# Optimization experiments

Measured on AMD Instinct MI355X. Metric: run time of the kernel, lower is better.

## Reference

```python
import jax, jax.numpy as jnp
import numpy as np

# ---- model constants (match init_kwargs) ----
E = 128; GH = 8; GD = E // GH; GL = 3          # graph emb / heads / layers
SH = 4; SD = E // SH; SL = 4                   # sequence transformer
ATOM = 64; BOND = 16; RBF_K = 32; CUTOFF = 5.0
VOCAB = 64; SEQL = 128
N = 32                                          # nodes per graph (equal-size graphs)
GC = 64; GS = 16; BMOL = 16; DEG = 64; GF = 3   # conf graphs / scaffold graphs / molecules / edges-per-graph
LN_EPS = 1e-5
CENTERS = jnp.linspace(0.0, CUTOFF, RBF_K)
GAMMA = (CUTOFF / (RBF_K - 1)) ** -2            # GaussianRBF gamma = (center spacing)^-2


def _ln(x, g, b):
    mu = x.mean(-1, keepdims=True)
    var = ((x - mu) ** 2).mean(-1, keepdims=True)
    return (x - mu) / jnp.sqrt(var + LN_EPS) * g + b


def _graph_encoder(x, edge_index, edge_attr, pos, G, p):
    # node projection
    h = x @ p["gproj_w"] + p["gproj_b"]                      # [G*N, E]
    # edge features: bond features + RBF(distance)
    d = jnp.clip(edge_attr[:, -1], 0.0, 10.0)
    rbf = jnp.exp(-GAMMA * (d[:, None] - CENTERS) ** 2)       # [M, K]
    ef = jnp.concatenate([edge_attr[:, :-1], rbf], axis=1)    # [M, BOND+K]
    # EdgeNetwork: per-edge matrix (gather -> matvec -> scatter-add)
    M = ef.shape[0]
    m = (ef @ p["elin_w"] + p["elin_b"]).reshape(M, E, E)
    msg = jnp.einsum("mef,mf->me", m, h[edge_index[1]])      # [M, E]
    aggr = jnp.zeros_like(h).at[edge_index[0]].add(msg)
    h = _ln(h + aggr, p["eln_g"], p["eln_b"])
    # dense per-graph layout (equal-size graphs -> reshape, mask is all-true)
    hb = h.reshape(G, N, E)
    pp = pos.reshape(G, N, 3)
    d2 = jnp.sum((pp[:, :, None, :] - pp[:, None, :, :]) ** 2, axis=-1)
    dist = jnp.where(d2 > 0, jnp.sqrt(jnp.where(d2 > 0, d2, 1.0)), 0.0)  # safe cdist
    inv_sqrt_d = 1.0 / np.sqrt(GD)
    for l in range(GL):
        def heads(t):
            return t.reshape(G, N, GH, GD).transpose(0, 2, 1, 3)
        q = heads(hb @ p["gt_qw"][l] + p["gt_qb"][l])
        k = heads(hb @ p["gt_kw"][l] + p["gt_kb"][l])
        v = heads(hb @ p["gt_vw"][l] + p["gt_vb"][l])
        s = jnp.einsum("bhnd,bhmd->bhnm", q, k) * inv_sqrt_d + dist[:, None]
        s = jnp.clip(s, -10.0, 10.0)
        a = jax.nn.softmax(s, axis=-1)                       # all nodes valid -> no mask
        o = jnp.einsum("bhnm,bhmd->bhnd", a, v).transpose(0, 2, 1, 3).reshape(G, N, E)
        o = o @ p["gt_ow"][l] + p["gt_ob"][l]
        x1 = _ln(hb + o, p["gt_ln1g"][l], p["gt_ln1b"][l])
        ff = jax.nn.relu(x1 @ p["gt_f1w"][l] + p["gt_f1b"][l]) @ p["gt_f2w"][l] + p["gt_f2b"][l]
        hb = _ln(x1 + ff, p["gt_ln2g"][l], p["gt_ln2b"][l])
    # masked mean pool with the source's eps in the denominator
    return hb.sum(1) / (N + 1e-8)


def _seq_encoder(tokens, p):
    B, L = tokens.shape
    x = p["tok_emb"][tokens] + p["pos_emb"][:L][None]        # [B, L, E]
    inv_sqrt_d = 1.0 / np.sqrt(SD)
    for l in range(SL):
        qkv = x @ p["se_inw"][l] + p["se_inb"][l]            # [B, L, 3E]
        q, k, v = jnp.split(qkv, 3, axis=-1)
        def heads(t):
            return t.reshape(B, L, SH, SD).transpose(0, 2, 1, 3)
        q, k, v = heads(q), heads(k), heads(v)
        a = jax.nn.softmax(jnp.einsum("bhnd,bhmd->bhnm", q, k) * inv_sqrt_d, axis=-1)
        o = jnp.einsum("bhnm,bhmd->bhnd", a, v).transpose(0, 2, 1, 3).reshape(B, L, E)
        o = o @ p["se_ow"][l] + p["se_ob"][l]
        x = _ln(x + o, p["se_ln1g"][l], p["se_ln1b"][l])      # post-norm (torch default)
        ff = jax.nn.relu(x @ p["se_f1w"][l] + p["se_f1b"][l]) @ p["se_f2w"][l] + p["se_f2b"][l]
        x = _ln(x + ff, p["se_ln2g"][l], p["se_ln2b"][l])
    return x.mean(1)                                          # [B, E]


def _forward(p, conf_edge_index, scaf_edge_index, tokens, conf_per_mol):
    g_all = _graph_encoder(p["conf_x"], conf_edge_index, p["conf_edge_attr"], p["conf_pos"], GC, p)
    conf_emb = g_all.reshape(-1, conf_per_mol, E).mean(1)     # per-molecule conformer mean (equal counts)
    scaf_emb = _graph_encoder(p["scaf_x"], scaf_edge_index, p["scaf_edge_attr"], p["scaf_pos"], GS, p)
    total = conf_emb + scaf_emb
    seq = _seq_encoder(tokens, p)
    # FusionGating
    gate_h = jax.nn.relu(jnp.concatenate([total, seq], -1) @ p["fg1_w"] + p["fg1_b"])
    gate = jax.nn.sigmoid(gate_h @ p["fg2_w"] + p["fg2_b"])
    fused = gate * total + (1.0 - gate) * seq
    # CrossModalAttention: MHA over a length-1 sequence (unsqueeze(0)) -> softmax
    # weights are identically 1, so attn(q_in, kv, kv) == out_proj(v_proj(kv)).
    g, s = fused, fused
    for l in range(2):
        g2s = (s @ p["cm_g2s_vw"][l] + p["cm_g2s_vb"][l]) @ p["cm_g2s_ow"][l] + p["cm_g2s_ob"][l]
        g = _ln(g + g2s, p["cm_n1g"][l], p["cm_n1b"][l])
        s2g = (g @ p["cm_s2g_vw"][l] + p["cm_s2g_vb"][l]) @ p["cm_s2g_ow"][l] + p["cm_s2g_ob"][l]
        s = _ln(s + s2g, p["cm_n2g"][l], p["cm_n2b"][l])
    final = (g + s) * 0.5
    comb = jnp.concatenate([final, p["graph_features"]], -1)
    return (jax.nn.relu(comb @ p["r1_w"] + p["r1_b"]) @ p["r2_w"] + p["r2_b"])[:, 0]


def setup_inputs() -> dict:
    ks = iter(jax.random.split(jax.random.key(0), 64))
    def nrm(shape, s):
        return (jax.random.normal(next(ks), shape) * s).astype(jnp.float32)
    inp = {}
    def mk_graph(prefix, G):
        inp[prefix + "_x"] = nrm((G * N, ATOM), 1.0)
        off = (jnp.arange(G) * N)[:, None]
        src = jax.random.randint(next(ks), (G, DEG), 0, N) + off   # within-graph edges
        dst = jax.random.randint(next(ks), (G, DEG), 0, N) + off
        inp[prefix + "_edge_index"] = jnp.stack([src.ravel(), dst.ravel()]).astype(jnp.int32)
        bond = jax.random.uniform(next(ks), (G * DEG, BOND))
        dist = jax.random.uniform(next(ks), (G * DEG, 1), minval=0.5, maxval=CUTOFF)
        inp[prefix + "_edge_attr"] = jnp.concatenate([bond, dist], 1).astype(jnp.float32)
        inp[prefix + "_pos"] = nrm((G * N, 3), 2.0)
    mk_graph("conf", GC)
    mk_graph("scaf", GS)
    inp["tokens"] = jax.random.randint(next(ks), (BMOL, SEQL), 1, VOCAB).astype(jnp.int32)
    inp["graph_features"] = nrm((BMOL, GF), 1.0)
    inp["conf_per_mol"] = GC // BMOL
    W = 0.05
    inp["gproj_w"] = nrm((ATOM, E), W); inp["gproj_b"] = jnp.zeros(E)
    inp["elin_w"] = nrm((BOND + RBF_K, E * E), W); inp["elin_b"] = jnp.zeros(E * E)
    inp["eln_g"] = jnp.ones(E); inp["eln_b"] = jnp.zeros(E)
    for nm in ["qw", "kw", "vw", "ow"]:
        inp["gt_" + nm] = nrm((GL, E, E), W)
        inp["gt_" + nm[0] + "b"] = jnp.zeros((GL, E))
    inp["gt_ln1g"] = jnp.ones((GL, E)); inp["gt_ln1b"] = jnp.zeros((GL, E))
    inp["gt_f1w"] = nrm((GL, E, 2 * E), W); inp["gt_f1b"] = jnp.zeros((GL, 2 * E))
    inp["gt_f2w"] = nrm((GL, 2 * E, E), W); inp["gt_f2b"] = jnp.zeros((GL, E))
    inp["gt_ln2g"] = jnp.ones((GL, E)); inp["gt_ln2b"] = jnp.zeros((GL, E))
    inp["tok_emb"] = nrm((VOCAB, E), 0.02); inp["pos_emb"] = nrm((256, E), 0.02)
    inp["se_inw"] = nrm((SL, E, 3 * E), W); inp["se_inb"] = jnp.zeros((SL, 3 * E))
    inp["se_ow"] = nrm((SL, E, E), W); inp["se_ob"] = jnp.zeros((SL, E))
    inp["se_ln1g"] = jnp.ones((SL, E)); inp["se_ln1b"] = jnp.zeros((SL, E))
    inp["se_f1w"] = nrm((SL, E, 2 * E), W); inp["se_f1b"] = jnp.zeros((SL, 2 * E))
    inp["se_f2w"] = nrm((SL, 2 * E, E), W); inp["se_f2b"] = jnp.zeros((SL, E))
    inp["se_ln2g"] = jnp.ones((SL, E)); inp["se_ln2b"] = jnp.zeros((SL, E))
    inp["fg1_w"] = nrm((2 * E, 64), W); inp["fg1_b"] = jnp.zeros(64)
    inp["fg2_w"] = nrm((64, E), W); inp["fg2_b"] = jnp.zeros(E)
    for nm in ["g2s", "s2g"]:
        inp["cm_" + nm + "_vw"] = nrm((2, E, E), W); inp["cm_" + nm + "_vb"] = jnp.zeros((2, E))
        inp["cm_" + nm + "_ow"] = nrm((2, E, E), W); inp["cm_" + nm + "_ob"] = jnp.zeros((2, E))
    inp["cm_n1g"] = jnp.ones((2, E)); inp["cm_n1b"] = jnp.zeros((2, E))
    inp["cm_n2g"] = jnp.ones((2, E)); inp["cm_n2b"] = jnp.zeros((2, E))
    inp["r1_w"] = nrm((E + GF, E), W); inp["r1_b"] = jnp.zeros(E)
    inp["r2_w"] = nrm((E, 1), W); inp["r2_b"] = jnp.zeros(1)
    return inp


def reference(conf_x, conf_edge_attr, conf_pos, scaf_x, scaf_edge_attr, scaf_pos, graph_features,
              gproj_w, gproj_b, elin_w, elin_b, eln_g, eln_b,
              gt_qw, gt_qb, gt_kw, gt_kb, gt_vw, gt_vb, gt_ow, gt_ob,
              gt_ln1g, gt_ln1b, gt_f1w, gt_f1b, gt_f2w, gt_f2b, gt_ln2g, gt_ln2b,
              tok_emb, pos_emb,
              se_inw, se_inb, se_ow, se_ob, se_ln1g, se_ln1b, se_f1w, se_f1b, se_f2w, se_f2b, se_ln2g, se_ln2b,
              fg1_w, fg1_b, fg2_w, fg2_b,
              cm_g2s_vw, cm_g2s_vb, cm_g2s_ow, cm_g2s_ob, cm_n1g, cm_n1b,
              cm_s2g_vw, cm_s2g_vb, cm_s2g_ow, cm_s2g_ob, cm_n2g, cm_n2b,
              r1_w, r1_b, r2_w, r2_b,
              conf_edge_index, scaf_edge_index, tokens, conf_per_mol):
    p = dict(locals())
    return _forward(p, conf_edge_index, scaf_edge_index, tokens, conf_per_mol)
```

## Files before the change

kernel.cpp:

```cpp
#include <hip/hip_runtime.h>
#include <hip/hip_bf16.h>


__device__ __forceinline__ float blk_norm(float v, int e, float* sred)
{
  float s = v;
  #pragma unroll
  for (int o = 1; o < 64; o <<= 1) s += __shfl_xor(s, o);
  if ((e & 63) == 0) sred[e >> 6] = s;
  __syncthreads();
  float mean = (sred[0] + sred[1]) * (1.0f / 128.0f);
  __syncthreads();
  float d = v - mean;
  float s2 = d * d;
  #pragma unroll
  for (int o = 1; o < 64; o <<= 1) s2 += __shfl_xor(s2, o);
  if ((e & 63) == 0) sred[e >> 6] = s2;
  __syncthreads();
  float var = (sred[0] + sred[1]) * (1.0f / 128.0f);
  __syncthreads();
  return d / sqrtf(var + 1e-5f);
}

__global__ __launch_bounds__(128) void node_proj_k(
    const float* __restrict__ cx, const float* __restrict__ sx,
    const float* __restrict__ w, const float* __restrict__ b,
    float* __restrict__ h, float* __restrict__ aggr)
{
  int r = blockIdx.x, e = threadIdx.x;
  const float* x = (r < 2048) ? (cx + (size_t)r * 64) : (sx + (size_t)(r - 2048) * 64);
  __shared__ float xs[64];
  if (e < 64) xs[e] = x[e];
  __syncthreads();
  float acc = b[e];
  for (int a = 0; a < 64; a++) acc += xs[a] * w[a * 128 + e];
  h[(size_t)r * 128 + e] = acc;
  aggr[(size_t)r * 128 + e] = 0.0f;
}

__global__ __launch_bounds__(256) void dist_k(
    const float* __restrict__ cpos, const float* __restrict__ spos, float* __restrict__ dist)
{
  int g = blockIdx.x, tid = threadIdx.x;
  __shared__ float P[96];
  const float* p = (g < 64) ? (cpos + (size_t)g * 96) : (spos + (size_t)(g - 64) * 96);
  if (tid < 96) P[tid] = p[tid];
  __syncthreads();
  #pragma unroll
  for (int jj = 0; jj < 4; jj++) {
    int idx = tid * 4 + jj;
    int i = idx >> 5, j = idx & 31;
    float dx = P[i * 3 + 0] - P[j * 3 + 0];
    float dy = P[i * 3 + 1] - P[j * 3 + 1];
    float dz = P[i * 3 + 2] - P[j * 3 + 2];
    float d2 = dx * dx + dy * dy + dz * dz;
    dist[(size_t)g * 1024 + idx] = (d2 > 0.0f) ? sqrtf(d2) : 0.0f;
  }
}

__global__ __launch_bounds__(256) void edge_gemm_k(
    const float* __restrict__ cea, const float* __restrict__ sea,
    const int* __restrict__ cei, const int* __restrict__ sei,
    const float* __restrict__ h,
    const float* __restrict__ elw, const float* __restrict__ elb,
    float* __restrict__ aggr)
{
  __shared__ float efs[32][8];
  __shared__ float As[32][36];
  __shared__ float Bs[32][136];
  const int tid = threadIdx.x;
  const int m0 = blockIdx.x * 32;
  const int kt0 = blockIdx.y * 28;
  const int c0 = kt0 >> 2;
  {
    int t = tid >> 3, cc = tid & 7;
    if (cc < 7) {
      int c = c0 + cc;
      int m = m0 + t;
      const float* attr = (m < 4096) ? (cea + (size_t)m * 17) : (sea + (size_t)(m - 4096) * 17);
      float val;
      if (c < 16) val = attr[c];
      else if (c < 48) {
        float d = fminf(fmaxf(attr[16], 0.0f), 10.0f);
        float t2 = d - (float)((c - 16) * (5.0 / 31.0));
        val = expf(-38.44f * t2 * t2);
      } else val = 1.0f;
      efs[t][cc] = val;
    }
  }
  const int gk = tid & 31, gt = (tid >> 5) * 4;
  float hreg[4][4];
  #pragma unroll
  for (int i = 0; i < 4; i++) {
    int m = m0 + gt + i;
    int dst = (m < 4096) ? cei[4096 + m] : (sei[1024 + (m - 4096)] + 2048);
    const float* hp = h + (size_t)dst * 128 + gk;
    hreg[i][0] = hp[0]; hreg[i][1] = hp[32]; hreg[i][2] = hp[64]; hreg[i][3] = hp[96];
  }
  const int tn = tid & 31, tm = tid >> 5;
  const int e0 = 4 * tn, t0 = 4 * tm;
  const int se = tid >> 1, sk = (tid & 1) * 16;
  float acc[4][4] = {};
  __syncthreads();
  #pragma unroll 1
  for (int kt = kt0; kt < kt0 + 28; kt++) {
    int c = kt >> 2, cc = c - c0, j = kt & 3;
    float4 av;
    av.x = efs[gt + 0][cc] * hreg[0][j];
    av.y = efs[gt + 1][cc] * hreg[1][j];
    av.z = efs[gt + 2][cc] * hreg[2][j];
    av.w = efs[gt + 3][cc] * hreg[3][j];
    *(float4*)&As[gk][gt] = av;
    const float* bp = ((c < 48) ? (elw + (size_t)c * 16384) : elb) + (size_t)se * 128 + j * 32 + sk;
    float4 w0 = *(const float4*)(bp + 0);
    float4 w1 = *(const float4*)(bp + 4);
    float4 w2 = *(const float4*)(bp + 8);
    float4 w3 = *(const float4*)(bp + 12);
    Bs[sk + 0][se] = w0.x;  Bs[sk + 1][se] = w0.y;  Bs[sk + 2][se] = w0.z;  Bs[sk + 3][se] = w0.w;
    Bs[sk + 4][se] = w1.x;  Bs[sk + 5][se] = w1.y;  Bs[sk + 6][se] = w1.z;  Bs[sk + 7][se] = w1.w;
    Bs[sk + 8][se] = w2.x;  Bs[sk + 9][se] = w2.y;  Bs[sk + 10][se] = w2.z; Bs[sk + 11][se] = w2.w;
    Bs[sk + 12][se] = w3.x; Bs[sk + 13][se] = w3.y; Bs[sk + 14][se] = w3.z; Bs[sk + 15][se] = w3.w;
    __syncthreads();
    #pragma unroll
    for (int kk = 0; kk < 32; kk++) {
      float4 a = *(const float4*)&As[kk][t0];
      float4 b = *(const float4*)&Bs[kk][e0];
      acc[0][0] += a.x * b.x; acc[0][1] += a.x * b.y; acc[0][2] += a.x * b.z; acc[0][3] += a.x * b.w;
      acc[1][0] += a.y * b.x; acc[1][1] += a.y * b.y; acc[1][2] += a.y * b.z; acc[1][3] += a.y * b.w;
      acc[2][0] += a.z * b.x; acc[2][1] += a.z * b.y; acc[2][2] += a.z * b.z; acc[2][3] += a.z * b.w;
      acc[3][0] += a.w * b.x; acc[3][1] += a.w * b.y; acc[3][2] += a.w * b.z; acc[3][3] += a.w * b.w;
    }
    __syncthreads();
  }
  #pragma unroll
  for (int i = 0; i < 4; i++) {
    int m = m0 + t0 + i;
    int src = (m < 4096) ? cei[m] : (sei[m - 4096] + 2048);
    float* dst = aggr + (size_t)src * 128 + e0;
    atomicAdd(dst + 0, acc[i][0]);
    atomicAdd(dst + 1, acc[i][1]);
    atomicAdd(dst + 2, acc[i][2]);
    atomicAdd(dst + 3, acc[i][3]);
  }
}

__device__ __forceinline__ void gemm16_body(
    const float* __restrict__ A, const float* __restrict__ Bp,
    const float* __restrict__ biasp, float* __restrict__ Cp,
    int row0, int ldb, int ldc)
{
  __shared__ float Sa[32][20];
  __shared__ float Bs[32][136];
  const int tid = threadIdx.x;
  const int tm = tid >> 5, tn = tid & 31;
  const int t0 = 2 * tm, e0 = 4 * tn;
  const int ar = tid >> 4, ak = (tid & 15) * 2;
  const int bk = tid >> 3, be = (tid & 7) * 16;
  float acc[2][4] = {};
  for (int k0 = 0; k0 < 128; k0 += 32) {
    float2 av = *(const float2*)(A + (size_t)(row0 + ar) * 128 + k0 + ak);
    Sa[ak][ar] = av.x; Sa[ak + 1][ar] = av.y;
    const float* bp = Bp + (size_t)(k0 + bk) * ldb + be;
    float4 b0v = *(const float4*)(bp + 0);
    float4 b1v = *(const float4*)(bp + 4);
    float4 b2v = *(const float4*)(bp + 8);
    float4 b3v = *(const float4*)(bp + 12);
    Bs[bk][be + 0] = b0v.x;  Bs[bk][be + 1] = b0v.y;  Bs[bk][be + 2] = b0v.z;  Bs[bk][be + 3] = b0v.w;
    Bs[bk][be + 4] = b1v.x;  Bs[bk][be + 5] = b1v.y;  Bs[bk][be + 6] = b1v.z;  Bs[bk][be + 7] = b1v.w;
    Bs[bk][be + 8] = b2v.x;  Bs[bk][be + 9] = b2v.y;  Bs[bk][be + 10] = b2v.z; Bs[bk][be + 11] = b2v.w;
    Bs[bk][be + 12] = b3v.x; Bs[bk][be + 13] = b3v.y; Bs[bk][be + 14] = b3v.z; Bs[bk][be + 15] = b3v.w;
    __syncthreads();
    #pragma unroll
    for (int kk = 0; kk < 32; kk++) {
      float2 a = *(const float2*)&Sa[kk][t0];
      float4 b = *(const float4*)&Bs[kk][e0];
      acc[0][0] += a.x * b.x; acc[0][1] += a.x * b.y; acc[0][2] += a.x * b.z; acc[0][3] += a.x * b.w;
      acc[1][0] += a.y * b.x; acc[1][1] += a.y * b.y; acc[1][2] += a.y * b.z; acc[1][3] += a.y * b.w;
    }
    __syncthreads();
  }
  #pragma unroll
  for (int i = 0; i < 2; i++) {
    float* cp = Cp + (size_t)(row0 + t0 + i) * ldc + e0;
    #pragma unroll
    for (int j = 0; j < 4; j++) cp[j] = acc[i][j] + biasp[e0 + j];
  }
}

__global__ __launch_bounds__(256) void qkv_k(
    int gBlocks,
    const float* __restrict__ ghb,
    const float* gqw, const float* gkw, const float* gvw,
    const float* gqb, const float* gkb, const float* gvb, float* gout,
    const float* __restrict__ sxs, const float* sw, const float* sb, float* sout)
{
  int bx = blockIdx.x;
  if (bx < gBlocks) {
    int z = bx / 160, rt = bx % 160;
    const float* B = (z == 0) ? gqw : (z == 1) ? gkw : gvw;
    const float* bias = (z == 0) ? gqb : (z == 1) ? gkb : gvb;
    gemm16_body(ghb, B, bias, gout + (size_t)z * 327680, rt * 16, 128, 128);
  } else {
    int i = bx - gBlocks;
    int z = i >> 7, rt = i & 127;
    gemm16_body(sxs, sw + z * 128, sb + z * 128, sout + z * 128, rt * 16, 384, 384);
  }
}

__device__ __forceinline__ void gattn_body(
    int g, int h, const float* __restrict__ q, const float* __restrict__ k,
    const float* __restrict__ v, const float* __restrict__ dist, float* __restrict__ o)
{
  __shared__ float qs[32][17], ksh[32][17], vsh[32][17], ss[32][33], rs[32];
  const int tid = threadIdx.x;
  {
    int idx = tid * 2;
    int i = idx >> 4, d = idx & 15;
    size_t base = ((size_t)(g * 32 + i)) * 128 + h * 16 + d;
    qs[i][d] = q[base];  qs[i][d + 1] = q[base + 1];
    ksh[i][d] = k[base]; ksh[i][d + 1] = k[base + 1];
    vsh[i][d] = v[base]; vsh[i][d + 1] = v[base + 1];
  }
  __syncthreads();
  {
    int i = tid >> 3, j0 = (tid & 7) * 4;
    for (int j = j0; j < j0 + 4; j++) {
      float a = 0;
      #pragma unroll
      for (int d = 0; d < 16; d++) a += qs[i][d] * ksh[j][d];
      a = a * 0.25f + dist[(size_t)g * 1024 + i * 32 + j];
      ss[i][j] = fminf(fmaxf(a, -10.0f), 10.0f);
    }
  }
  __syncthreads();
  if (tid < 32) {
    float m = -1e30f;
    for (int j = 0; j < 32; j++) m = fmaxf(m, ss[tid][j]);
    float sm = 0;
    for (int j = 0; j < 32; j++) { float ex = expf(ss[tid][j] - m); ss[tid][j] = ex; sm += ex; }
    rs[tid] = 1.0f / sm;
  }
  __syncthreads();
  {
    int idx = tid * 2;
    int i = idx >> 4, d = idx & 15;
    float a0 = 0, a1 = 0;
    for (int j = 0; j < 32; j++) { float wj = ss[i][j]; a0 += wj * vsh[j][d]; a1 += wj * vsh[j][d + 1]; }
    float r = rs[i];
    size_t base = ((size_t)(g * 32 + i)) * 128 + h * 16 + d;
    o[base] = a0 * r; o[base + 1] = a1 * r;
  }
}

__device__ __forceinline__ void sattn_body(
    int b, int h, int qt, const float* __restrict__ qkv, float* __restrict__ o)
{
  __shared__ float ks[128][33];
  __shared__ float vs[128][33];
  __shared__ float qs2[32][33];
  __shared__ float ss2[32][129];
  __shared__ float red[32][8];
  __shared__ float red2[32][8];
  const int tid = threadIdx.x;
  {
    int l = tid >> 1, d0 = (tid & 1) * 16;
    const float* kp = qkv + ((size_t)(b * 128 + l)) * 384 + 128 + h * 32 + d0;
    #pragma unroll
    for (int j = 0; j < 16; j++) { ks[l][d0 + j] = kp[j]; vs[l][d0 + j] = kp[128 + j]; }
  }
  {
    int i = tid >> 3, d0 = (tid & 7) * 4;
    const float* qp = qkv + ((size_t)(b * 128 + qt * 32 + i)) * 384 + h * 32 + d0;
    #pragma unroll
    for (int j = 0; j < 4; j++) qs2[i][d0 + j] = qp[j];
  }
  __syncthreads();
  const int i = tid >> 3, sub = tid & 7;
  {
    int j0 = sub * 16;
    for (int j = j0; j < j0 + 16; j++) {
      float a = 0;
      #pragma unroll
      for (int d = 0; d < 32; d++) a += qs2[i][d] * ks[j][d];
      ss2[i][j] = a * 0.17677669529663687f;
    }
  }
  __syncthreads();
  float m = -1e30f;
  for (int j = sub; j < 128; j += 8) m = fmaxf(m, ss2[i][j]);
  red[i][sub] = m;
  __syncthreads();
  float mm = red[i][0];
  #pragma unroll
  for (int t = 1; t < 8; t++) mm = fmaxf(mm, red[i][t]);
  float ps = 0;
  for (int j = sub; j < 128; j += 8) { float ex = expf(ss2[i][j] - mm); ss2[i][j] = ex; ps += ex; }
  red2[i][sub] = ps;
  __syncthreads();
  float sm = 0;
  #pragma unroll
  for (int t = 0; t < 8; t++) sm += red2[i][t];
  float rinv = 1.0f / sm;
  {
    int d0 = sub * 4;
    float a0 = 0, a1 = 0, a2 = 0, a3 = 0;
    for (int j = 0; j < 128; j++) {
      float wj = ss2[i][j];
      a0 += wj * vs[j][d0 + 0]; a1 += wj * vs[j][d0 + 1];
      a2 += wj * vs[j][d0 + 2]; a3 += wj * vs[j][d0 + 3];
    }
    float* op = o + ((size_t)(b * 128 + qt * 32 + i)) * 128 + h * 32 + d0;
    op[0] = a0 * rinv; op[1] = a1 * rinv; op[2] = a2 * rinv; op[3] = a3 * rinv;
  }
}

__global__ __launch_bounds__(256) void attn_k(
    int gBlocks, const float* q, const float* k, const float* v,
    const float* dist, float* go, const float* qkv, float* so)
{
  int bx = blockIdx.x;
  if (bx < gBlocks) gattn_body(bx >> 3, bx & 7, q, k, v, dist, go);
  else { int i = bx - gBlocks; sattn_body(i >> 4, (i >> 2) & 3, i & 3, qkv, so); }
}

__device__ __forceinline__ void tail_body(
    int row0, const float* __restrict__ A,
    const float* __restrict__ Wo, const float* __restrict__ bo, const float* __restrict__ res,
    const float* __restrict__ g1, const float* __restrict__ b1n,
    const float* __restrict__ W1, const float* __restrict__ b1f,
    const float* __restrict__ W2, const float* __restrict__ b2f,
    const float* __restrict__ g2, const float* __restrict__ b2n,
    float* __restrict__ Out)
{
  __shared__ float x1[16][132];
  __shared__ float hid[16][260];
  __shared__ __align__(16) float sbuf[4352];
  __shared__ float Sa[32][20];
  float (*BsA)[136] = (float(*)[136])sbuf;
  float (*Bs1)[260] = (float(*)[260])sbuf;
  float (*Bs2)[136] = (float(*)[136])sbuf;
  const int tid = threadIdx.x;
  {
    const int tm = tid >> 5, tn = tid & 31;
    const int t0 = 2 * tm, e0 = 4 * tn;
    const int ar = tid >> 4, ak = (tid & 15) * 2;
    const int bk = tid >> 3, be = (tid & 7) * 16;
    float acc[2][4] = {};
    for (int k0 = 0; k0 < 128; k0 += 32) {
      float2 av = *(const float2*)(A + (size_t)(row0 + ar) * 128 + k0 + ak);
      Sa[ak][ar] = av.x; Sa[ak + 1][ar] = av.y;
      const float* bp = Wo + (size_t)(k0 + bk) * 128 + be;
      float4 b0v = *(const float4*)(bp + 0);
      float4 b1v = *(const float4*)(bp + 4);
      float4 b2v = *(const float4*)(bp + 8);
      float4 b3v = *(const float4*)(bp + 12);
      BsA[bk][be + 0] = b0v.x;  BsA[bk][be + 1] = b0v.y;  BsA[bk][be + 2] = b0v.z;  BsA[bk][be + 3] = b0v.w;
      BsA[bk][be + 4] = b1v.x;  BsA[bk][be + 5] = b1v.y;  BsA[bk][be + 6] = b1v.z;  BsA[bk][be + 7] = b1v.w;
      BsA[bk][be + 8] = b2v.x;  BsA[bk][be + 9] = b2v.y;  BsA[bk][be + 10] = b2v.z; BsA[bk][be + 11] = b2v.w;
      BsA[bk][be + 12] = b3v.x; BsA[bk][be + 13] = b3v.y; BsA[bk][be + 14] = b3v.z; BsA[bk][be + 15] = b3v.w;
      __syncthreads();
      #pragma unroll
      for (int kk = 0; kk < 32; kk++) {
        float2 a = *(const float2*)&Sa[kk][t0];
        float4 b = *(const float4*)&BsA[kk][e0];
        acc[0][0] += a.x * b.x; acc[0][1] += a.x * b.y; acc[0][2] += a.x * b.z; acc[0][3] += a.x * b.w;
        acc[1][0] += a.y * b.x; acc[1][1] += a.y * b.y; acc[1][2] += a.y * b.z; acc[1][3] += a.y * b.w;
      }
      __syncthreads();
    }
    #pragma unroll
    for (int i = 0; i < 2; i++) {
      int r = row0 + t0 + i;
      float v0 = acc[i][0] + bo[e0 + 0] + res[(size_t)r * 128 + e0 + 0];
      float v1 = acc[i][1] + bo[e0 + 1] + res[(size_t)r * 128 + e0 + 1];
      float v2 = acc[i][2] + bo[e0 + 2] + res[(size_t)r * 128 + e0 + 2];
      float v3 = acc[i][3] + bo[e0 + 3] + res[(size_t)r * 128 + e0 + 3];
      float s = v0 + v1 + v2 + v3;
      #pragma unroll
      for (int o = 1; o < 32; o <<= 1) s += __shfl_xor(s, o);
      float mean = s * (1.0f / 128.0f);
      float d0 = v0 - mean, d1 = v1 - mean, d2 = v2 - mean, d3 = v3 - mean;
      float sq = d0 * d0 + d1 * d1 + d2 * d2 + d3 * d3;
      #pragma unroll
      for (int o = 1; o < 32; o <<= 1) sq += __shfl_xor(sq, o);
      float rstd = 1.0f / sqrtf(sq * (1.0f / 128.0f) + 1e-5f);
      x1[t0 + i][e0 + 0] = d0 * rstd * g1[e0 + 0] + b1n[e0 + 0];
      x1[t0 + i][e0 + 1] = d1 * rstd * g1[e0 + 1] + b1n[e0 + 1];
      x1[t0 + i][e0 + 2] = d2 * rstd * g1[e0 + 2] + b1n[e0 + 2];
      x1[t0 + i][e0 + 3] = d3 * rstd * g1[e0 + 3] + b1n[e0 + 3];
    }
  }
  __syncthreads();
  {
    const int tm = tid >> 6, tn = tid & 63;
    const int t0 = 4 * tm, e0 = 4 * tn;
    const int ar = tid >> 4, ak = tid & 15;
    const int bk = tid >> 4, be = (tid & 15) * 16;
    float acc[4][4] = {};
    for (int k0 = 0; k0 < 128; k0 += 16) {
      Sa[ak][ar] = x1[ar][k0 + ak];
      const float* bp = W1 + (size_t)(k0 + bk) * 256 + be;
      float4 b0v = *(const float4*)(bp + 0);
      float4 b1v = *(const float4*)(bp + 4);
      float4 b2v = *(const float4*)(bp + 8);
      float4 b3v = *(const float4*)(bp + 12);
      Bs1[bk][be + 0] = b0v.x;  Bs1[bk][be + 1] = b0v.y;  Bs1[bk][be + 2] = b0v.z;  Bs1[bk][be + 3] = b0v.w;
      Bs1[bk][be + 4] = b1v.x;  Bs1[bk][be + 5] = b1v.y;  Bs1[bk][be + 6] = b1v.z;  Bs1[bk][be + 7] = b1v.w;
      Bs1[bk][be + 8] = b2v.x;  Bs1[bk][be + 9] = b2v.y;  Bs1[bk][be + 10] = b2v.z; Bs1[bk][be + 11] = b2v.w;
      Bs1[bk][be + 12] = b3v.x; Bs1[bk][be + 13] = b3v.y; Bs1[bk][be + 14] = b3v.z; Bs1[bk][be + 15] = b3v.w;
      __syncthreads();
      #pragma unroll
      for (int kk = 0; kk < 16; kk++) {
        float4 a = *(const float4*)&Sa[kk][t0];
        float4 b = *(const float4*)&Bs1[kk][e0];
        acc[0][0] += a.x * b.x; acc[0][1] += a.x * b.y; acc[0][2] += a.x * b.z; acc[0][3] += a.x * b.w;
        acc[1][0] += a.y * b.x; acc[1][1] += a.y * b.y; acc[1][2] += a.y * b.z; acc[1][3] += a.y * b.w;
        acc[2][0] += a.z * b.x; acc[2][1] += a.z * b.y; acc[2][2] += a.z * b.z; acc[2][3] += a.z * b.w;
        acc[3][0] += a.w * b.x; acc[3][1] += a.w * b.y; acc[3][2] += a.w * b.z; acc[3][3] += a.w * b.w;
      }
      __syncthreads();
    }
    #pragma unroll
    for (int i = 0; i < 4; i++) {
      float4 hv;
      hv.x = fmaxf(acc[i][0] + b1f[e0 + 0], 0.0f);
      hv.y = fmaxf(acc[i][1] + b1f[e0 + 1], 0.0f);
      hv.z = fmaxf(acc[i][2] + b1f[e0 + 2], 0.0f);
      hv.w = fmaxf(acc[i][3] + b1f[e0 + 3], 0.0f);
      *(float4*)&hid[t0 + i][e0] = hv;
    }
  }
  __syncthreads();
  {
    const int tm = tid >> 5, tn = tid & 31;
    const int t0 = 2 * tm, e0 = 4 * tn;
    const int bk = tid >> 3, be = (tid & 7) * 16;
    float acc[2][4] = {};
    for (int k0 = 0; k0 < 256; k0 += 32) {
      const float* bp = W2 + (size_t)(k0 + bk) * 128 + be;
      float4 b0v = *(const float4*)(bp + 0);
      float4 b1v = *(const float4*)(bp + 4);
      float4 b2v = *(const float4*)(bp + 8);
      float4 b3v = *(const float4*)(bp + 12);
      Bs2[bk][be + 0] = b0v.x;  Bs2[bk][be + 1] = b0v.y;  Bs2[bk][be + 2] = b0v.z;  Bs2[bk][be + 3] = b0v.w;
      Bs2[bk][be + 4] = b1v.x;  Bs2[bk][be + 5] = b1v.y;  Bs2[bk][be + 6] = b1v.z;  Bs2[bk][be + 7] = b1v.w;
      Bs2[bk][be + 8] = b2v.x;  Bs2[bk][be + 9] = b2v.y;  Bs2[bk][be + 10] = b2v.z; Bs2[bk][be + 11] = b2v.w;
      Bs2[bk][be + 12] = b3v.x; Bs2[bk][be + 13] = b3v.y; Bs2[bk][be + 14] = b3v.z; Bs2[bk][be + 15] = b3v.w;
      __syncthreads();
      #pragma unroll
      for (int kk = 0; kk < 32; kk++) {
        float a0 = hid[t0 + 0][k0 + kk];
        float a1 = hid[t0 + 1][k0 + kk];
        float4 b = *(const float4*)&Bs2[kk][e0];
        acc[0][0] += a0 * b.x; acc[0][1] += a0 * b.y; acc[0][2] += a0 * b.z; acc[0][3] += a0 * b.w;
        acc[1][0] += a1 * b.x; acc[1][1] += a1 * b.y; acc[1][2] += a1 * b.z; acc[1][3] += a1 * b.w;
      }
      __syncthreads();
    }
    #pragma unroll
    for (int i = 0; i < 2; i++) {
      int r = row0 + t0 + i;
      float v0 = acc[i][0] + b2f[e0 + 0] + x1[t0 + i][e0 + 0];
      float v1 = acc[i][1] + b2f[e0 + 1] + x1[t0 + i][e0 + 1];
      float v2 = acc[i][2] + b2f[e0 + 2] + x1[t0 + i][e0 + 2];
      float v3 = acc[i][3] + b2f[e0 + 3] + x1[t0 + i][e0 + 3];
      float s = v0 + v1 + v2 + v3;
      #pragma unroll
      for (int o = 1; o < 32; o <<= 1) s += __shfl_xor(s, o);
      float mean = s * (1.0f / 128.0f);
      float d0 = v0 - mean, d1 = v1 - mean, d2 = v2 - mean, d3 = v3 - mean;
      float sq = d0 * d0 + d1 * d1 + d2 * d2 + d3 * d3;
      #pragma unroll
      for (int o = 1; o < 32; o <<= 1) sq += __shfl_xor(sq, o);
      float rstd = 1.0f / sqrtf(sq * (1.0f / 128.0f) + 1e-5f);
      float* cp = Out + (size_t)r * 128 + e0;
      cp[0] = d0 * rstd * g2[e0 + 0] + b2n[e0 + 0];
      cp[1] = d1 * rstd * g2[e0 + 1] + b2n[e0 + 1];
      cp[2] = d2 * rstd * g2[e0 + 2] + b2n[e0 + 2];
      cp[3] = d3 * rstd * g2[e0 + 3] + b2n[e0 + 3];
    }
  }
}

__global__ __launch_bounds__(256) void tail_k(
    int gBlocks,
    const float* gA, const float* gWo, const float* gbo, const float* gres,
    const float* gg1, const float* gb1, const float* gW1, const float* gbf1,
    const float* gW2, const float* gbf2, const float* gg2, const float* gb2, float* gOut,
    const float* sA, const float* sWo, const float* sbo, const float* sres,
    const float* sg1, const float* sb1, const float* sW1, const float* sbf1,
    const float* sW2, const float* sbf2, const float* sg2, const float* sb2, float* sOut)
{
  int bx = blockIdx.x;
  if (bx < gBlocks)
    tail_body(bx * 16, gA, gWo, gbo, gres, gg1, gb1, gW1, gbf1, gW2, gbf2, gg2, gb2, gOut);
  else
    tail_body((bx - gBlocks) * 16, sA, sWo, sbo, sres, sg1, sb1, sW1, sbf1, sW2, sbf2, sg2, sb2, sOut);
}

__global__ __launch_bounds__(128) void ln_k(
    const float* __restrict__ x, const float* __restrict__ res,
    const float* __restrict__ g, const float* __restrict__ b, float* __restrict__ out)
{
  __shared__ float sred[2];
  int r = blockIdx.x, e = threadIdx.x;
  size_t idx = (size_t)r * 128 + e;
  float v = x[idx] + res[idx];
  float nv = blk_norm(v, e, sred);
  out[idx] = nv * g[e] + b[e];
}

__global__ __launch_bounds__(128) void embed_k(
    const int* __restrict__ tokens, const float* __restrict__ tok_emb,
    const float* __restrict__ pos_emb, float* __restrict__ xs)
{
  int r = blockIdx.x, e = threadIdx.x;
  int tk = tokens[r];
  xs[(size_t)r * 128 + e] = tok_emb[(size_t)tk * 128 + e] + pos_emb[(size_t)(r & 127) * 128 + e];
}

__global__ __launch_bounds__(128) void head_k(
    const float* __restrict__ hb, const float* __restrict__ xs, const float* __restrict__ gfeat,
    const float* fg1w, const float* fg1b, const float* fg2w, const float* fg2b,
    const float* g2s_vw, const float* g2s_vb, const float* g2s_ow, const float* g2s_ob,
    const float* n1g, const float* n1b,
    const float* s2g_vw, const float* s2g_vb, const float* s2g_ow, const float* s2g_ob,
    const float* n2g, const float* n2b,
    const float* r1w, const float* r1b, const float* r2w, const float* r2b,
    float* __restrict__ out)
{
  __shared__ float T[128], S[128], G[128], Sm[128], t1[128], t2[128], gh[64], sred[2];
  int mol = blockIdx.x, e = threadIdx.x;
  {
    float cs = 0;
    for (int c = 0; c < 4; c++) {
      int g = mol * 4 + c;
      float s = 0;
      for (int i = 0; i < 32; i++) s += hb[((size_t)(g * 32 + i)) * 128 + e];
      cs += s * (1.0f / 32.0f);
    }
    cs *= 0.25f;
    float s2 = 0;
    int g = 64 + mol;
    for (int i = 0; i < 32; i++) s2 += hb[((size_t)(g * 32 + i)) * 128 + e];
    T[e] = cs + s2 * (1.0f / 32.0f);
    float ss = 0;
    for (int l = 0; l < 128; l++) ss += xs[((size_t)(mol * 128 + l)) * 128 + e];
    S[e] = ss * (1.0f / 128.0f);
  }
  __syncthreads();
  if (e < 64) {
    float a = fg1b[e];
    for (int f = 0; f < 128; f++) a += T[f] * fg1w[f * 64 + e];
    for (int f = 0; f < 128; f++) a += S[f] * fg1w[(128 + f) * 64 + e];
    gh[e] = fmaxf(a, 0.0f);
  }
  __syncthreads();
  {
    float a = fg2b[e];
    for (int j = 0; j < 64; j++) a += gh[j] * fg2w[j * 128 + e];
    float gate = 1.0f / (1.0f + expf(-a));
    float fu = gate * T[e] + (1.0f - gate) * S[e];
    G[e] = fu; Sm[e] = fu;
  }
  __syncthreads();
  for (int l = 0; l < 2; l++) {
    const float* vw = g2s_vw + (size_t)l * 16384; const float* vb = g2s_vb + l * 128;
    const float* ow = g2s_ow + (size_t)l * 16384; const float* ob = g2s_ob + l * 128;
    float a = vb[e];
    for (int f = 0; f < 128; f++) a += Sm[f] * vw[f * 128 + e];
    t1[e] = a;
    __syncthreads();
    a = ob[e];
    for (int f = 0; f < 128; f++) a += t1[f] * ow[f * 128 + e];
    float nv = blk_norm(G[e] + a, e, sred);
    G[e] = nv * n1g[l * 128 + e] + n1b[l * 128 + e];
    __syncthreads();
    const float* vw2 = s2g_vw + (size_t)l * 16384; const float* vb2 = s2g_vb + l * 128;
    const float* ow2 = s2g_ow + (size_t)l * 16384; const float* ob2 = s2g_ob + l * 128;
    a = vb2[e];
    for (int f = 0; f < 128; f++) a += G[f] * vw2[f * 128 + e];
    t1[e] = a;
    __syncthreads();
    a = ob2[e];
    for (int f = 0; f < 128; f++) a += t1[f] * ow2[f * 128 + e];
    nv = blk_norm(Sm[e] + a, e, sred);
    Sm[e] = nv * n2g[l * 128 + e] + n2b[l * 128 + e];
    __syncthreads();
  }
  t2[e] = 0.5f * (G[e] + Sm[e]);
  __syncthreads();
  float a = r1b[e];
  for (int f = 0; f < 128; f++) a += t2[f] * r1w[f * 128 + e];
  for (int f = 0; f < 3; f++) a += gfeat[mol * 3 + f] * r1w[(128 + f) * 128 + e];
  a = fmaxf(a, 0.0f);
  float p = a * r2w[e];
  #pragma unroll
  for (int o = 1; o < 64; o <<= 1) p += __shfl_xor(p, o);
  if ((e & 63) == 0) sred[e >> 6] = p;
  __syncthreads();
  if (e == 0) out[mol] = sred[0] + sred[1] + r2b[0];
}

extern "C" void kernel_launch(void* const* d_in, const int* in_sizes, int n_in,
                              void* d_out, int out_size, void* d_ws, size_t ws_size,
                              hipStream_t stream)
{
  (void)n_in; (void)out_size; (void)ws_size;
  const bool dict = (in_sizes[1] == 8192);
  auto IN = [&](int di, int si) { return d_in[dict ? di : si]; };

  const float* conf_x   = (const float*)IN(0, 0);
  const int*   conf_ei  = (const int*)  IN(1, 63);
  const float* conf_ea  = (const float*)IN(2, 1);
  const float* conf_pos = (const float*)IN(3, 2);
  const float* scaf_x   = (const float*)IN(4, 3);
  const int*   scaf_ei  = (const int*)  IN(5, 64);
  const float* scaf_ea  = (const float*)IN(6, 4);
  const float* scaf_pos = (const float*)IN(7, 5);
  const int*   tokens   = (const int*)  IN(8, 65);
  const float* gfeat    = (const float*)IN(9, 6);
  const float* gproj_w  = (const float*)IN(11, 7);
  const float* gproj_b  = (const float*)IN(12, 8);
  const float* elin_w   = (const float*)IN(13, 9);
  const float* elin_b   = (const float*)IN(14, 10);
  const float* eln_g    = (const float*)IN(15, 11);
  const float* eln_b    = (const float*)IN(16, 12);
  const float* gt_qw    = (const float*)IN(17, 13);
  const float* gt_qb    = (const float*)IN(18, 14);
  const float* gt_kw    = (const float*)IN(19, 15);
  const float* gt_kb    = (const float*)IN(20, 16);
  const float* gt_vw    = (const float*)IN(21, 17);
  const float* gt_vb    = (const float*)IN(22, 18);
  const float* gt_ow    = (const float*)IN(23, 19);
  const float* gt_ob    = (const float*)IN(24, 20);
  const float* gt_ln1g  = (const float*)IN(25, 21);
  const float* gt_ln1b  = (const float*)IN(26, 22);
  const float* gt_f1w   = (const float*)IN(27, 23);
  const float* gt_f1b   = (const float*)IN(28, 24);
  const float* gt_f2w   = (const float*)IN(29, 25);
  const float* gt_f2b   = (const float*)IN(30, 26);
  const float* gt_ln2g  = (const float*)IN(31, 27);
  const float* gt_ln2b  = (const float*)IN(32, 28);
  const float* tok_emb  = (const float*)IN(33, 29);
  const float* pos_emb  = (const float*)IN(34, 30);
  const float* se_inw   = (const float*)IN(35, 31);
  const float* se_inb   = (const float*)IN(36, 32);
  const float* se_ow    = (const float*)IN(37, 33);
  const float* se_ob    = (const float*)IN(38, 34);
  const float* se_ln1g  = (const float*)IN(39, 35);
  const float* se_ln1b  = (const float*)IN(40, 36);
  const float* se_f1w   = (const float*)IN(41, 37);
  const float* se_f1b   = (const float*)IN(42, 38);
  const float* se_f2w   = (const float*)IN(43, 39);
  const float* se_f2b   = (const float*)IN(44, 40);
  const float* se_ln2g  = (const float*)IN(45, 41);
  const float* se_ln2b  = (const float*)IN(46, 42);
  const float* fg1_w    = (const float*)IN(47, 43);
  const float* fg1_b    = (const float*)IN(48, 44);
  const float* fg2_w    = (const float*)IN(49, 45);
  const float* fg2_b    = (const float*)IN(50, 46);
  const float* cm_g2s_vw = (const float*)IN(51, 47);
  const float* cm_g2s_vb = (const float*)IN(52, 48);
  const float* cm_g2s_ow = (const float*)IN(53, 49);
  const float* cm_g2s_ob = (const float*)IN(54, 50);
  const float* cm_s2g_vw = (const float*)IN(55, 53);
  const float* cm_s2g_vb = (const float*)IN(56, 54);
  const float* cm_s2g_ow = (const float*)IN(57, 55);
  const float* cm_s2g_ob = (const float*)IN(58, 56);
  const float* cm_n1g   = (const float*)IN(59, 51);
  const float* cm_n1b   = (const float*)IN(60, 52);
  const float* cm_n2g   = (const float*)IN(61, 57);
  const float* cm_n2b   = (const float*)IN(62, 58);
  const float* r1_w     = (const float*)IN(63, 59);
  const float* r1_b     = (const float*)IN(64, 60);
  const float* r2_w     = (const float*)IN(65, 61);
  const float* r2_b     = (const float*)IN(66, 62);
  float* out = (float*)d_out;

  float* w = (float*)d_ws;
  size_t off = 0;
  auto alloc = [&](size_t n) { float* p = w + off; off += n; return p; };
  float* h     = alloc(2560 * 128);
  float* aggr  = alloc(2560 * 128);
  float* hb    = alloc(2560 * 128);
  float* distb = alloc(80 * 1024);
  float* qb    = alloc(3 * 327680);
  float* atto  = alloc(327680);
  float* xs2   = alloc(2048 * 128);
  float* qkv3  = alloc(2048 * 384);
  float* satto = alloc(2048 * 128);
  float* xsfin = alloc(2048 * 128);

  node_proj_k<<<2560, 128, 0, stream>>>(conf_x, scaf_x, gproj_w, gproj_b, h, aggr);
  dist_k<<<80, 256, 0, stream>>>(conf_pos, scaf_pos, distb);
  edge_gemm_k<<<dim3(160, 7), 256, 0, stream>>>(conf_ea, scaf_ea, conf_ei, scaf_ei, h, elin_w, elin_b, aggr);
  ln_k<<<2560, 128, 0, stream>>>(aggr, h, eln_g, eln_b, hb);
  embed_k<<<2048, 128, 0, stream>>>(tokens, tok_emb, pos_emb, xs2);

  for (int l = 0; l < 4; l++) {
    const bool hasG = (l < 3);
    const int lg = hasG ? l : 0;
    const int gq = hasG ? 480 : 0;
    const int ga = hasG ? 640 : 0;
    const int gt = hasG ? 160 : 0;
    float* sOut = (l == 3) ? xsfin : xs2;
    qkv_k<<<gq + 384, 256, 0, stream>>>(gq,
        hb, gt_qw + (size_t)lg * 16384, gt_kw + (size_t)lg * 16384, gt_vw + (size_t)lg * 16384,
        gt_qb + lg * 128, gt_kb + lg * 128, gt_vb + lg * 128, qb,
        xs2, se_inw + (size_t)l * 49152, se_inb + l * 384, qkv3);
    attn_k<<<ga + 256, 256, 0, stream>>>(ga, qb, qb + 327680, qb + 655360, distb, atto, qkv3, satto);
    tail_k<<<gt + 128, 256, 0, stream>>>(gt,
        atto, gt_ow + (size_t)lg * 16384, gt_ob + lg * 128, hb,
        gt_ln1g + lg * 128, gt_ln1b + lg * 128,
        gt_f1w + (size_t)lg * 32768, gt_f1b + lg * 256,
        gt_f2w + (size_t)lg * 32768, gt_f2b + lg * 128,
        gt_ln2g + lg * 128, gt_ln2b + lg * 128, hb,
        satto, se_ow + (size_t)l * 16384, se_ob + l * 128, xs2,
        se_ln1g + l * 128, se_ln1b + l * 128,
        se_f1w + (size_t)l * 32768, se_f1b + l * 256,
        se_f2w + (size_t)l * 32768, se_f2b + l * 128,
        se_ln2g + l * 128, se_ln2b + l * 128, sOut);
  }

  head_k<<<16, 128, 0, stream>>>(hb, xsfin, gfeat,
                                 fg1_w, fg1_b, fg2_w, fg2_b,
                                 cm_g2s_vw, cm_g2s_vb, cm_g2s_ow, cm_g2s_ob, cm_n1g, cm_n1b,
                                 cm_s2g_vw, cm_s2g_vb, cm_s2g_ow, cm_s2g_ob, cm_n2g, cm_n2b,
                                 r1_w, r1_b, r2_w, r2_b, out);
}
```

Measured before the change: 663.6 us.

## Fuse front-end kernels and double edge GEMM tile to 64 edges

Node projection, pairwise distance and token embedding kernels are merged into one launch using block-index ranges, which saves two kernel launches. The edge GEMM now handles 64 edges per block with a 4x8 register tile per thread, so each weight tile loaded into shared memory is reused across twice as many edges and the weight traffic halves. The cost is higher register pressure and only 560 blocks, down from 1120, which may leave some of the GPU's compute units underfilled.

```diff
diff --git a/kernel.cpp b/kernel.cpp
--- a/kernel.cpp
+++ b/kernel.cpp
@@ -22,39 +22,45 @@
   return d / sqrtf(var + 1e-5f);
 }
 
-__global__ __launch_bounds__(128) void node_proj_k(
+__global__ __launch_bounds__(256) void front_k(
     const float* __restrict__ cx, const float* __restrict__ sx,
     const float* __restrict__ w, const float* __restrict__ b,
-    float* __restrict__ h, float* __restrict__ aggr)
-{
-  int r = blockIdx.x, e = threadIdx.x;
-  const float* x = (r < 2048) ? (cx + (size_t)r * 64) : (sx + (size_t)(r - 2048) * 64);
-  __shared__ float xs[64];
-  if (e < 64) xs[e] = x[e];
-  __syncthreads();
-  float acc = b[e];
-  for (int a = 0; a < 64; a++) acc += xs[a] * w[a * 128 + e];
-  h[(size_t)r * 128 + e] = acc;
-  aggr[(size_t)r * 128 + e] = 0.0f;
-}
-
-__global__ __launch_bounds__(256) void dist_k(
-    const float* __restrict__ cpos, const float* __restrict__ spos, float* __restrict__ dist)
-{
-  int g = blockIdx.x, tid = threadIdx.x;
-  __shared__ float P[96];
-  const float* p = (g < 64) ? (cpos + (size_t)g * 96) : (spos + (size_t)(g - 64) * 96);
-  if (tid < 96) P[tid] = p[tid];
-  __syncthreads();
-  #pragma unroll
-  for (int jj = 0; jj < 4; jj++) {
-    int idx = tid * 4 + jj;
-    int i = idx >> 5, j = idx & 31;
-    float dx = P[i * 3 + 0] - P[j * 3 + 0];
-    float dy = P[i * 3 + 1] - P[j * 3 + 1];
-    float dz = P[i * 3 + 2] - P[j * 3 + 2];
-    float d2 = dx * dx + dy * dy + dz * dz;
-    dist[(size_t)g * 1024 + idx] = (d2 > 0.0f) ? sqrtf(d2) : 0.0f;
+    float* __restrict__ h, float* __restrict__ aggr,
+    const float* __restrict__ cpos, const float* __restrict__ spos, float* __restrict__ dist,
+    const int* __restrict__ tokens, const float* __restrict__ tok_emb,
+    const float* __restrict__ pos_emb, float* __restrict__ xs)
+{
+  __shared__ float sP[128];
+  const int bx = blockIdx.x, tid = threadIdx.x;
+  if (bx < 1280) {
+    int r = bx * 2 + (tid >> 7), e = tid & 127;
+    const float* x = (r < 2048) ? (cx + (size_t)r * 64) : (sx + (size_t)(r - 2048) * 64);
+    float* xrow = sP + (tid >> 7) * 64;
+    if (e < 64) xrow[e] = x[e];
+    __syncthreads();
+    float acc = b[e];
+    for (int a = 0; a < 64; a++) acc += xrow[a] * w[a * 128 + e];
+    h[(size_t)r * 128 + e] = acc;
+    aggr[(size_t)r * 128 + e] = 0.0f;
+  } else if (bx < 1360) {
+    int g = bx - 1280;
+    const float* p = (g < 64) ? (cpos + (size_t)g * 96) : (spos + (size_t)(g - 64) * 96);
+    if (tid < 96) sP[tid] = p[tid];
+    __syncthreads();
+    #pragma unroll
+    for (int jj = 0; jj < 4; jj++) {
+      int idx = tid * 4 + jj;
+      int i = idx >> 5, j = idx & 31;
+      float dx = sP[i * 3 + 0] - sP[j * 3 + 0];
+      float dy = sP[i * 3 + 1] - sP[j * 3 + 1];
+      float dz = sP[i * 3 + 2] - sP[j * 3 + 2];
+      float d2 = dx * dx + dy * dy + dz * dz;
+      dist[(size_t)g * 1024 + idx] = (d2 > 0.0f) ? sqrtf(d2) : 0.0f;
+    }
+  } else {
+    int r = (bx - 1360) * 2 + (tid >> 7), e = tid & 127;
+    int tk = tokens[r];
+    xs[(size_t)r * 128 + e] = tok_emb[(size_t)tk * 128 + e] + pos_emb[(size_t)(r & 127) * 128 + e];
   }
 }
 
@@ -65,15 +71,15 @@
     const float* __restrict__ elw, const float* __restrict__ elb,
     float* __restrict__ aggr)
 {
-  __shared__ float efs[32][8];
-  __shared__ float As[32][36];
+  __shared__ float efs[64][8];
+  __shared__ float As[32][68];
   __shared__ float Bs[32][136];
   const int tid = threadIdx.x;
-  const int m0 = blockIdx.x * 32;
+  const int m0 = blockIdx.x * 64;
   const int kt0 = blockIdx.y * 28;
   const int c0 = kt0 >> 2;
-  {
-    int t = tid >> 3, cc = tid & 7;
+  for (int i = tid; i < 512; i += 256) {
+    int t = i >> 3, cc = i & 7;
     if (cc < 7) {
       int c = c0 + cc;
       int m = m0 + t;
@@ -88,29 +94,34 @@
       efs[t][cc] = val;
     }
   }
-  const int gk = tid & 31, gt = (tid >> 5) * 4;
-  float hreg[4][4];
+  const int gk = tid & 31, g8 = tid >> 5;
+  float hreg[8][4];
   #pragma unroll
-  for (int i = 0; i < 4; i++) {
-    int m = m0 + gt + i;
+  for (int i = 0; i < 8; i++) {
+    int m = m0 + g8 * 8 + i;
     int dst = (m < 4096) ? cei[4096 + m] : (sei[1024 + (m - 4096)] + 2048);
     const float* hp = h + (size_t)dst * 128 + gk;
     hreg[i][0] = hp[0]; hreg[i][1] = hp[32]; hreg[i][2] = hp[64]; hreg[i][3] = hp[96];
   }
-  const int tn = tid & 31, tm = tid >> 5;
-  const int e0 = 4 * tn, t0 = 4 * tm;
+  const int tn = tid & 15, tm = tid >> 4;
+  const int e0 = 8 * tn, t0 = 4 * tm;
   const int se = tid >> 1, sk = (tid & 1) * 16;
-  float acc[4][4] = {};
+  float acc[4][8] = {};
   __syncthreads();
   #pragma unroll 1
   for (int kt = kt0; kt < kt0 + 28; kt++) {
     int c = kt >> 2, cc = c - c0, j = kt & 3;
-    float4 av;
-    av.x = efs[gt + 0][cc] * hreg[0][j];
-    av.y = efs[gt + 1][cc] * hreg[1][j];
-    av.z = efs[gt + 2][cc] * hreg[2][j];
-    av.w = efs[gt + 3][cc] * hreg[3][j];
-    *(float4*)&As[gk][gt] = av;
+    float4 a0, a1;
+    a0.x = efs[g8 * 8 + 0][cc] * hreg[0][j];
+    a0.y = efs[g8 * 8 + 1][cc] * hreg[1][j];
+    a0.z = efs[g8 * 8 + 2][cc] * hreg[2][j];
+    a0.w = efs[g8 * 8 + 3][cc] * hreg[3][j];
+    a1.x = efs[g8 * 8 + 4][cc] * hreg[4][j];
+    a1.y = efs[g8 * 8 + 5][cc] * hreg[5][j];
+    a1.z = efs[g8 * 8 + 6][cc] * hreg[6][j];
+    a1.w = efs[g8 * 8 + 7][cc] * hreg[7][j];
+    *(float4*)&As[gk][g8 * 8] = a0;
+    *(float4*)&As[gk][g8 * 8 + 4] = a1;
     const float* bp = ((c < 48) ? (elw + (size_t)c * 16384) : elb) + (size_t)se * 128 + j * 32 + sk;
     float4 w0 = *(const float4*)(bp + 0);
     float4 w1 = *(const float4*)(bp + 4);
@@ -124,11 +135,16 @@
     #pragma unroll
     for (int kk = 0; kk < 32; kk++) {
       float4 a = *(const float4*)&As[kk][t0];
-      float4 b = *(const float4*)&Bs[kk][e0];
-      acc[0][0] += a.x * b.x; acc[0][1] += a.x * b.y; acc[0][2] += a.x * b.z; acc[0][3] += a.x * b.w;
-      acc[1][0] += a.y * b.x; acc[1][1] += a.y * b.y; acc[1][2] += a.y * b.z; acc[1][3] += a.y * b.w;
-      acc[2][0] += a.z * b.x; acc[2][1] += a.z * b.y; acc[2][2] += a.z * b.z; acc[2][3] += a.z * b.w;
-      acc[3][0] += a.w * b.x; acc[3][1] += a.w * b.y; acc[3][2] += a.w * b.z; acc[3][3] += a.w * b.w;
+      float4 b0 = *(const float4*)&Bs[kk][e0];
+      float4 b1 = *(const float4*)&Bs[kk][e0 + 4];
+      acc[0][0] += a.x * b0.x; acc[0][1] += a.x * b0.y; acc[0][2] += a.x * b0.z; acc[0][3] += a.x * b0.w;
+      acc[0][4] += a.x * b1.x; acc[0][5] += a.x * b1.y; acc[0][6] += a.x * b1.z; acc[0][7] += a.x * b1.w;
+      acc[1][0] += a.y * b0.x; acc[1][1] += a.y * b0.y; acc[1][2] += a.y * b0.z; acc[1][3] += a.y * b0.w;
+      acc[1][4] += a.y * b1.x; acc[1][5] += a.y * b1.y; acc[1][6] += a.y * b1.z; acc[1][7] += a.y * b1.w;
+      acc[2][0] += a.z * b0.x; acc[2][1] += a.z * b0.y; acc[2][2] += a.z * b0.z; acc[2][3] += a.z * b0.w;
+      acc[2][4] += a.z * b1.x; acc[2][5] += a.z * b1.y; acc[2][6] += a.z * b1.z; acc[2][7] += a.z * b1.w;
+      acc[3][0] += a.w * b0.x; acc[3][1] += a.w * b0.y; acc[3][2] += a.w * b0.z; acc[3][3] += a.w * b0.w;
+      acc[3][4] += a.w * b1.x; acc[3][5] += a.w * b1.y; acc[3][6] += a.w * b1.z; acc[3][7] += a.w * b1.w;
     }
     __syncthreads();
   }
@@ -137,10 +153,8 @@
     int m = m0 + t0 + i;
     int src = (m < 4096) ? cei[m] : (sei[m - 4096] + 2048);
     float* dst = aggr + (size_t)src * 128 + e0;
-    atomicAdd(dst + 0, acc[i][0]);
-    atomicAdd(dst + 1, acc[i][1]);
-    atomicAdd(dst + 2, acc[i][2]);
-    atomicAdd(dst + 3, acc[i][3]);
+    #pragma unroll
+    for (int j = 0; j < 8; j++) atomicAdd(dst + j, acc[i][j]);
   }
 }
 
@@ -508,15 +522,6 @@
   float v = x[idx] + res[idx];
   float nv = blk_norm(v, e, sred);
   out[idx] = nv * g[e] + b[e];
-}
-
-__global__ __launch_bounds__(128) void embed_k(
-    const int* __restrict__ tokens, const float* __restrict__ tok_emb,
-    const float* __restrict__ pos_emb, float* __restrict__ xs)
-{
-  int r = blockIdx.x, e = threadIdx.x;
-  int tk = tokens[r];
-  xs[(size_t)r * 128 + e] = tok_emb[(size_t)tk * 128 + e] + pos_emb[(size_t)(r & 127) * 128 + e];
 }
 
 __global__ __launch_bounds__(128) void head_k(
@@ -692,11 +697,11 @@
   float* satto = alloc(2048 * 128);
   float* xsfin = alloc(2048 * 128);
 
-  node_proj_k<<<2560, 128, 0, stream>>>(conf_x, scaf_x, gproj_w, gproj_b, h, aggr);
-  dist_k<<<80, 256, 0, stream>>>(conf_pos, scaf_pos, distb);
-  edge_gemm_k<<<dim3(160, 7), 256, 0, stream>>>(conf_ea, scaf_ea, conf_ei, scaf_ei, h, elin_w, elin_b, aggr);
+  front_k<<<2384, 256, 0, stream>>>(conf_x, scaf_x, gproj_w, gproj_b, h, aggr,
+                                    conf_pos, scaf_pos, distb,
+                                    tokens, tok_emb, pos_emb, xs2);
+  edge_gemm_k<<<dim3(80, 7), 256, 0, stream>>>(conf_ea, scaf_ea, conf_ei, scaf_ei, h, elin_w, elin_b, aggr);
   ln_k<<<2560, 128, 0, stream>>>(aggr, h, eln_g, eln_b, hb);
-  embed_k<<<2048, 128, 0, stream>>>(tokens, tok_emb, pos_emb, xs2);
 
   for (int l = 0; l < 4; l++) {
     const bool hasG = (l < 3);
```

After: 765.6 us. +15.4%, slower.
